# Kernel tuning notes

Hardware: AMD Instinct MI355X
Metric: run time of the kernel (lower is better)

## Reference

```python
import jax, jax.numpy as jnp
import numpy as np

B, C, H, W = 4, 256, 64, 64
D = C // 8  # query/key projection dim


def setup_inputs() -> dict:
    key = jax.random.key(0)
    ks = jax.random.split(key, 8)
    s = 0.02
    return {
        "x": jax.random.normal(ks[0], (B, C, H, W), dtype=jnp.float32),
        "Wq": jax.random.normal(ks[1], (D, C), dtype=jnp.float32) * s,
        "bq": jax.random.normal(ks[2], (D,), dtype=jnp.float32) * s,
        "Wk": jax.random.normal(ks[3], (D, C), dtype=jnp.float32) * s,
        "bk": jax.random.normal(ks[4], (D,), dtype=jnp.float32) * s,
        "Wv": jax.random.normal(ks[5], (C, C), dtype=jnp.float32) * s,
        "bv": jax.random.normal(ks[6], (C,), dtype=jnp.float32) * s,
        "gamma": jax.random.normal(ks[7], (1,), dtype=jnp.float32),
    }


def reference(x, Wq, bq, Wk, bk, Wv, bv, gamma):
    b, c, h, w = x.shape
    n = h * w
    xf = x.reshape(b, c, n)                                  # B,C,N
    # 1x1 convs == per-pixel linear projections
    q = jnp.einsum("dc,bcn->bdn", Wq, xf) + bq[None, :, None]  # B,D,N
    k = jnp.einsum("dc,bcn->bdn", Wk, xf) + bk[None, :, None]  # B,D,N
    v = jnp.einsum("ec,bcn->ben", Wv, xf) + bv[None, :, None]  # B,C,N
    # energy[b,i,j] = <q[:, i], k[:, j]>  (query index i, key index j)
    energy = jnp.einsum("bdi,bdj->bij", q, k)                # B,N,N
    attention = jax.nn.softmax(energy, axis=-1)              # softmax over keys j
    # out[b,c,i] = sum_j v[b,c,j] * attention[b,i,j]
    out = jnp.einsum("bcj,bij->bci", v, attention)           # B,C,N
    out = out.reshape(b, c, h, w)
    return gamma[0] * out + x
```

## Files before the change

### kernel.cpp

```cpp
#include <hip/hip_runtime.h>
#include <hip/hip_bf16.h>
#include <cstdint>

#define B_ 4
#define C_ 256
#define N_ 4096
#define D_ 32

typedef __attribute__((ext_vector_type(8))) short bf16x8;
typedef __attribute__((ext_vector_type(4))) short s16x4;
typedef __attribute__((ext_vector_type(4))) float f32x4;

__device__ inline unsigned short f2bf(float f) {
    union { float f; uint32_t u; } v; v.f = f;
    uint32_t u = v.u;
    u += 0x7FFFu + ((u >> 16) & 1u);
    return (unsigned short)(u >> 16);
}

__global__ __launch_bounds__(256) void wconv_kernel(
    const float* __restrict__ Wq, const float* __restrict__ Wk,
    const float* __restrict__ Wv, unsigned short* __restrict__ Wb)
{
    int i = (blockIdx.x * 256 + threadIdx.x) * 4;
    int r = i >> 8, k = i & 255;
    const float* src = (r < 32) ? Wq + r * 256 + k
                     : (r < 64) ? Wk + (r - 32) * 256 + k
                                : Wv + (r - 64) * 256 + k;
    f32x4 v = *reinterpret_cast<const f32x4*>(src);
    s16x4 o;
    #pragma unroll
    for (int j = 0; j < 4; ++j) o[j] = (short)f2bf(v[j]);
    *reinterpret_cast<s16x4*>(Wb + i) = o;
}

__global__ __launch_bounds__(256) void proj_kernel(
    const float* __restrict__ x, const unsigned short* __restrict__ Wb,
    const float* __restrict__ bq, const float* __restrict__ bk,
    const float* __restrict__ bv,
    unsigned short* __restrict__ Qt, unsigned short* __restrict__ Kt,
    unsigned short* __restrict__ V)
{
    __shared__ __align__(16) char smem[32768];
    const int t  = threadIdx.x;
    const int w  = t >> 6;
    const int l  = t & 63;
    const int lg = l >> 4;
    const int ll = l & 15;
    const int n0 = blockIdx.x * 64;
    const int b  = blockIdx.y;

    #pragma unroll
    for (int rep = 0; rep < 16; ++rep) {
        int flat = rep * 256 + t;
        int c = flat >> 4, chunk = flat & 15;
        f32x4 xv = *reinterpret_cast<const f32x4*>(
            x + ((size_t)(b * C_ + c)) * N_ + n0 + chunk * 4);
        #pragma unroll
        for (int j = 0; j < 4; ++j) {
            int n = chunk * 4 + j;
            *reinterpret_cast<unsigned short*>(
                smem + n * 512 + ((c * 2) ^ ((n & 7) << 4))) = f2bf(xv[j]);
        }
    }

    bf16x8 Af[5], Afn[5];
    #pragma unroll
    for (int rt = 0; rt < 5; ++rt) {
        int r = w * 80 + rt * 16 + ll;
        Af[rt] = *reinterpret_cast<const bf16x8*>(Wb + r * 256 + lg * 8);
    }

    f32x4 acc[5][4];
    #pragma unroll
    for (int rt = 0; rt < 5; ++rt)
        #pragma unroll
        for (int nt = 0; nt < 4; ++nt) acc[rt][nt] = (f32x4){0.f, 0.f, 0.f, 0.f};

    __syncthreads();

    for (int kc = 0; kc < 8; ++kc) {
        if (kc < 7) {
            #pragma unroll
            for (int rt = 0; rt < 5; ++rt) {
                int r = w * 80 + rt * 16 + ll;
                Afn[rt] = *reinterpret_cast<const bf16x8*>(
                    Wb + r * 256 + (kc + 1) * 32 + lg * 8);
            }
        }
        bf16x8 Bf[4];
        #pragma unroll
        for (int nt = 0; nt < 4; ++nt) {
            int n = nt * 16 + ll;
            Bf[nt] = *reinterpret_cast<const bf16x8*>(
                smem + n * 512 + ((kc * 64 + lg * 16) ^ ((n & 7) << 4)));
        }
        #pragma unroll
        for (int rt = 0; rt < 5; ++rt)
            #pragma unroll
            for (int nt = 0; nt < 4; ++nt)
                acc[rt][nt] = __builtin_amdgcn_mfma_f32_16x16x32_bf16(
                    Af[rt], Bf[nt], acc[rt][nt], 0, 0, 0);
        if (kc < 7) {
            #pragma unroll
            for (int rt = 0; rt < 5; ++rt) Af[rt] = Afn[rt];
        }
    }

    #pragma unroll
    for (int rt = 0; rt < 5; ++rt) {
        const int rrow = w * 80 + rt * 16 + lg * 4;
        float bias[4];
        #pragma unroll
        for (int q = 0; q < 4; ++q) {
            int rg = rrow + q;
            bias[q] = (rg < 32) ? bq[rg] : (rg < 64) ? bk[rg - 32] : bv[rg - 64];
        }
        if (rrow < 64) {
            const int d0 = rrow & 31;
            unsigned short* dst = (rrow < 32) ? Qt : Kt;
            #pragma unroll
            for (int nt = 0; nt < 4; ++nt) {
                int n = n0 + nt * 16 + ll;
                s16x4 sv;
                #pragma unroll
                for (int q = 0; q < 4; ++q)
                    sv[q] = (short)f2bf(acc[rt][nt][q] + bias[q]);
                *reinterpret_cast<s16x4*>(dst + ((size_t)b * N_ + n) * D_ + d0) = sv;
            }
        } else {
            #pragma unroll
            for (int nt = 0; nt < 4; ++nt) {
                int n = n0 + nt * 16 + ll;
                #pragma unroll
                for (int q = 0; q < 4; ++q) {
                    int c = rrow - 64 + q;
                    V[((size_t)(b * C_ + c)) * N_ + n] = f2bf(acc[rt][nt][q] + bias[q]);
                }
            }
        }
    }
}

__device__ inline void stageV(const unsigned short* __restrict__ Vg, int b,
                              int c0, int j0, char* VsBuf, int w, int l) {
    #pragma unroll
    for (int i = 0; i < 2; ++i) {
        const int Lbyte = i * 8192 + w * 1024 + l * 16;
        const int c   = Lbyte >> 7;
        const int off = Lbyte & 127;
        const int src_off = off ^ ((c & 7) << 4);
        const unsigned short* src =
            Vg + ((size_t)(b * C_ + c0 + c)) * N_ + j0 + (src_off >> 1);
        char* dst = VsBuf + i * 8192 + w * 1024;
        __builtin_amdgcn_global_load_lds(
            (const __attribute__((address_space(1))) uint32_t*)src,
            (__attribute__((address_space(3))) uint32_t*)dst, 16, 0, 0);
    }
}

__global__ __launch_bounds__(512) void attn_kernel(
    const unsigned short* __restrict__ Qt, const unsigned short* __restrict__ Kt,
    const unsigned short* __restrict__ Vg, const float* __restrict__ x,
    const float* __restrict__ gamma, float* __restrict__ out)
{
    __shared__ __align__(16) char smem[49664];
    char* Pbase = smem + 32768;
    float* LbufF = reinterpret_cast<float*>(smem + 49152);
    const int t  = threadIdx.x;
    const int w  = t >> 6;
    const int l  = t & 63;
    const int lg = l >> 4;
    const int ll = l & 15;
    const int qg = w >> 2;
    const int ch = w & 3;
    const int qr = w >> 1;
    const int jcb = (w & 1) * 2;
    const int n0 = (blockIdx.x >> 1) * 64;
    const int c0 = (blockIdx.x & 1) * 128;
    const int b  = blockIdx.y;

    const bf16x8 qfrag = *reinterpret_cast<const bf16x8*>(
        Qt + ((size_t)b * N_ + n0 + qr * 16 + ll) * D_ + 8 * lg);

    f32x4 acc[2][2];
    #pragma unroll
    for (int qt = 0; qt < 2; ++qt)
        #pragma unroll
        for (int ct = 0; ct < 2; ++ct) acc[qt][ct] = (f32x4){0.f, 0.f, 0.f, 0.f};
    float l_lane[4] = {0.f, 0.f, 0.f, 0.f};

    stageV(Vg, b, c0, 0, smem, w, l);
    bf16x8 kcur[2], knxt[2];
    #pragma unroll
    for (int s = 0; s < 2; ++s)
        kcur[s] = *reinterpret_cast<const bf16x8*>(
            Kt + ((size_t)b * N_ + (jcb + s) * 16 + ll) * D_ + 8 * lg);

    const f32x4 zero4 = {0.f, 0.f, 0.f, 0.f};

    for (int kt = 0; kt < 64; ++kt) {
        const int buf = kt & 1;
        const int ktn = (kt < 63) ? kt + 1 : 63;

        #pragma unroll
        for (int s = 0; s < 2; ++s)
            knxt[s] = *reinterpret_cast<const bf16x8*>(
                Kt + ((size_t)b * N_ + ktn * 64 + (jcb + s) * 16 + ll) * D_ + 8 * lg);

        f32x4 sf[2];
        #pragma unroll
        for (int s = 0; s < 2; ++s)
            sf[s] = __builtin_amdgcn_mfma_f32_16x16x32_bf16(qfrag, kcur[s], zero4, 0, 0, 0);

        float pv[2][4];
        #pragma unroll
        for (int s = 0; s < 2; ++s)
            #pragma unroll
            for (int r = 0; r < 4; ++r) {
                float p = __expf(fminf(sf[s][r], 60.f));
                pv[s][r] = p;
                l_lane[r] += p;
            }

        char* Pw = Pbase + buf * 8192;
        #pragma unroll
        for (int s = 0; s < 2; ++s)
            #pragma unroll
            for (int r = 0; r < 4; ++r) {
                int row = qr * 16 + lg * 4 + r;
                int col = (jcb + s) * 16 + ll;
                *reinterpret_cast<unsigned short*>(
                    Pw + row * 128 + ((col * 2) ^ ((row & 7) << 4))) = f2bf(pv[s][r]);
            }

        asm volatile("s_waitcnt lgkmcnt(0)" ::: "memory");
        asm volatile("s_waitcnt vmcnt(2)" ::: "memory");
        __builtin_amdgcn_s_barrier();
        asm volatile("" ::: "memory");

        if (kt < 63)
            stageV(Vg, b, c0, ktn * 64, smem + (buf ^ 1) * 16384, w, l);

        char* Pr = Pbase + buf * 8192;
        bf16x8 pfrag[2][2];
        #pragma unroll
        for (int qt = 0; qt < 2; ++qt)
            #pragma unroll
            for (int kh = 0; kh < 2; ++kh) {
                int row = qg * 32 + qt * 16 + ll;
                pfrag[qt][kh] = *reinterpret_cast<const bf16x8*>(
                    Pr + row * 128 + ((kh * 64 + lg * 16) ^ ((row & 7) << 4)));
            }
        char* Vs = smem + buf * 16384;
        #pragma unroll
        for (int ct = 0; ct < 2; ++ct) {
            int cl = ch * 32 + ct * 16 + ll;
            #pragma unroll
            for (int kh = 0; kh < 2; ++kh) {
                bf16x8 vf = *reinterpret_cast<const bf16x8*>(
                    Vs + cl * 128 + ((kh * 64 + lg * 16) ^ ((cl & 7) << 4)));
                #pragma unroll
                for (int qt = 0; qt < 2; ++qt)
                    acc[qt][ct] = __builtin_amdgcn_mfma_f32_16x16x32_bf16(
                        pfrag[qt][kh], vf, acc[qt][ct], 0, 0, 0);
            }
        }

        #pragma unroll
        for (int s = 0; s < 2; ++s) kcur[s] = knxt[s];
    }

    #pragma unroll
    for (int off = 1; off < 16; off <<= 1)
        #pragma unroll
        for (int r = 0; r < 4; ++r)
            l_lane[r] += __shfl_xor(l_lane[r], off);
    if (ll == 0) {
        #pragma unroll
        for (int r = 0; r < 4; ++r) LbufF[w * 16 + lg * 4 + r] = l_lane[r];
    }
    __syncthreads();

    float inv[2][4];
    #pragma unroll
    for (int qt = 0; qt < 2; ++qt)
        #pragma unroll
        for (int r = 0; r < 4; ++r) {
            int qrow = qg * 2 + qt;
            int lq = lg * 4 + r;
            float ls = LbufF[(2 * qrow) * 16 + lq] + LbufF[(2 * qrow + 1) * 16 + lq];
            inv[qt][r] = 1.f / ls;
        }

    #pragma unroll
    for (int qt = 0; qt < 2; ++qt)
        #pragma unroll
        for (int ct = 0; ct < 2; ++ct) {
            int cl = ch * 32 + ct * 16 + ll;
            int ncol = qg * 32 + qt * 16 + lg * 4;
            f32x4 v;
            #pragma unroll
            for (int r = 0; r < 4; ++r) v[r] = acc[qt][ct][r] * inv[qt][r];
            *reinterpret_cast<f32x4*>(smem + cl * 256 + ((ncol * 4) ^ ((cl & 7) << 4))) = v;
        }
    __syncthreads();

    const float g0 = gamma[0];
    #pragma unroll
    for (int p = 0; p < 4; ++p) {
        int li = p * 512 + t;
        int cl = li >> 4;
        int n4 = (li & 15) * 4;
        f32x4 ov = *reinterpret_cast<const f32x4*>(
            smem + cl * 256 + ((n4 * 4) ^ ((cl & 7) << 4)));
        size_t gi = ((size_t)(b * C_ + c0 + cl)) * N_ + n0 + n4;
        f32x4 xv = *reinterpret_cast<const f32x4*>(x + gi);
        f32x4 res;
        #pragma unroll
        for (int j = 0; j < 4; ++j) res[j] = g0 * ov[j] + xv[j];
        *reinterpret_cast<f32x4*>(out + gi) = res;
    }
}

extern "C" void kernel_launch(void* const* d_in, const int* in_sizes, int n_in,
                              void* d_out, int out_size, void* d_ws, size_t ws_size,
                              hipStream_t stream) {
    const float* x     = (const float*)d_in[0];
    const float* Wq    = (const float*)d_in[1];
    const float* bq    = (const float*)d_in[2];
    const float* Wk    = (const float*)d_in[3];
    const float* bk    = (const float*)d_in[4];
    const float* Wv    = (const float*)d_in[5];
    const float* bv    = (const float*)d_in[6];
    const float* gamma = (const float*)d_in[7];
    float* out = (float*)d_out;

    char* ws = (char*)d_ws;
    unsigned short* Qt = (unsigned short*)(ws);
    unsigned short* Kt = (unsigned short*)(ws + (1u << 20));
    unsigned short* V  = (unsigned short*)(ws + (2u << 20));
    unsigned short* Wb = (unsigned short*)(ws + (10u << 20));

    wconv_kernel<<<dim3(80), 256, 0, stream>>>(Wq, Wk, Wv, Wb);
    proj_kernel<<<dim3(N_ / 64, B_), 256, 0, stream>>>(
        x, Wb, bq, bk, bv, Qt, Kt, V);
    attn_kernel<<<dim3(2 * N_ / 64, B_), 512, 0, stream>>>(
        Qt, Kt, V, x, gamma, out);
}
```

Baseline: 161.5 us.

## Retile attention to 32 queries by all channels, fold log2e into Q

The attention kernel now gives each block 32 query rows and all 256 channels instead of 64 queries and half the channels. QK^T and softmax are therefore computed once per query tile rather than twice, with each wave handling one 16-key column and 32 output channels. Q is prescaled by log2(e) in the projection so the softmax can use raw v_exp_f32, and the PV MFMA section runs under a raised s_setprio. The projection tile is halved to 32 pixels. In exchange, the attention kernel uses more LDS for the full-channel V double buffer, which may reduce occupancy.

```diff
diff --git a/kernel.cpp b/kernel.cpp
--- a/kernel.cpp
+++ b/kernel.cpp
@@ -6,6 +6,7 @@
 #define C_ 256
 #define N_ 4096
 #define D_ 32
+#define LOG2E 1.44269504088896f
 
 typedef __attribute__((ext_vector_type(8))) short bf16x8;
 typedef __attribute__((ext_vector_type(4))) short s16x4;
@@ -16,6 +17,12 @@
     uint32_t u = v.u;
     u += 0x7FFFu + ((u >> 16) & 1u);
     return (unsigned short)(u >> 16);
+}
+
+__device__ inline float exp2_raw(float x) {
+    float r;
+    asm("v_exp_f32 %0, %1" : "=v"(r) : "v"(x));
+    return r;
 }
 
 __global__ __launch_bounds__(256) void wconv_kernel(
@@ -41,19 +48,19 @@
     unsigned short* __restrict__ Qt, unsigned short* __restrict__ Kt,
     unsigned short* __restrict__ V)
 {
-    __shared__ __align__(16) char smem[32768];
+    __shared__ __align__(16) char smem[16384];
     const int t  = threadIdx.x;
     const int w  = t >> 6;
     const int l  = t & 63;
     const int lg = l >> 4;
     const int ll = l & 15;
-    const int n0 = blockIdx.x * 64;
+    const int n0 = blockIdx.x * 32;
     const int b  = blockIdx.y;
 
     #pragma unroll
-    for (int rep = 0; rep < 16; ++rep) {
+    for (int rep = 0; rep < 8; ++rep) {
         int flat = rep * 256 + t;
-        int c = flat >> 4, chunk = flat & 15;
+        int c = flat >> 3, chunk = flat & 7;
         f32x4 xv = *reinterpret_cast<const f32x4*>(
             x + ((size_t)(b * C_ + c)) * N_ + n0 + chunk * 4);
         #pragma unroll
@@ -71,11 +78,11 @@
         Af[rt] = *reinterpret_cast<const bf16x8*>(Wb + r * 256 + lg * 8);
     }
 
-    f32x4 acc[5][4];
+    f32x4 acc[5][2];
     #pragma unroll
     for (int rt = 0; rt < 5; ++rt)
         #pragma unroll
-        for (int nt = 0; nt < 4; ++nt) acc[rt][nt] = (f32x4){0.f, 0.f, 0.f, 0.f};
+        for (int nt = 0; nt < 2; ++nt) acc[rt][nt] = (f32x4){0.f, 0.f, 0.f, 0.f};
 
     __syncthreads();
 
@@ -88,9 +95,9 @@
                     Wb + r * 256 + (kc + 1) * 32 + lg * 8);
             }
         }
-        bf16x8 Bf[4];
-        #pragma unroll
-        for (int nt = 0; nt < 4; ++nt) {
+        bf16x8 Bf[2];
+        #pragma unroll
+        for (int nt = 0; nt < 2; ++nt) {
             int n = nt * 16 + ll;
             Bf[nt] = *reinterpret_cast<const bf16x8*>(
                 smem + n * 512 + ((kc * 64 + lg * 16) ^ ((n & 7) << 4)));
@@ -98,7 +105,7 @@
         #pragma unroll
         for (int rt = 0; rt < 5; ++rt)
             #pragma unroll
-            for (int nt = 0; nt < 4; ++nt)
+            for (int nt = 0; nt < 2; ++nt)
                 acc[rt][nt] = __builtin_amdgcn_mfma_f32_16x16x32_bf16(
                     Af[rt], Bf[nt], acc[rt][nt], 0, 0, 0);
         if (kc < 7) {
@@ -118,19 +125,23 @@
         }
         if (rrow < 64) {
             const int d0 = rrow & 31;
-            unsigned short* dst = (rrow < 32) ? Qt : Kt;
-            #pragma unroll
-            for (int nt = 0; nt < 4; ++nt) {
+            const bool isQ = (rrow < 32);
+            unsigned short* dst = isQ ? Qt : Kt;
+            #pragma unroll
+            for (int nt = 0; nt < 2; ++nt) {
                 int n = n0 + nt * 16 + ll;
                 s16x4 sv;
                 #pragma unroll
-                for (int q = 0; q < 4; ++q)
-                    sv[q] = (short)f2bf(acc[rt][nt][q] + bias[q]);
+                for (int q = 0; q < 4; ++q) {
+                    float v = acc[rt][nt][q] + bias[q];
+                    if (isQ) v *= LOG2E;
+                    sv[q] = (short)f2bf(v);
+                }
                 *reinterpret_cast<s16x4*>(dst + ((size_t)b * N_ + n) * D_ + d0) = sv;
             }
         } else {
             #pragma unroll
-            for (int nt = 0; nt < 4; ++nt) {
+            for (int nt = 0; nt < 2; ++nt) {
                 int n = n0 + nt * 16 + ll;
                 #pragma unroll
                 for (int q = 0; q < 4; ++q) {
@@ -143,15 +154,15 @@
 }
 
 __device__ inline void stageV(const unsigned short* __restrict__ Vg, int b,
-                              int c0, int j0, char* VsBuf, int w, int l) {
-    #pragma unroll
-    for (int i = 0; i < 2; ++i) {
+                              int j0, char* VsBuf, int w, int l) {
+    #pragma unroll
+    for (int i = 0; i < 4; ++i) {
         const int Lbyte = i * 8192 + w * 1024 + l * 16;
         const int c   = Lbyte >> 7;
         const int off = Lbyte & 127;
         const int src_off = off ^ ((c & 7) << 4);
         const unsigned short* src =
-            Vg + ((size_t)(b * C_ + c0 + c)) * N_ + j0 + (src_off >> 1);
+            Vg + ((size_t)(b * C_ + c)) * N_ + j0 + (src_off >> 1);
         char* dst = VsBuf + i * 8192 + w * 1024;
         __builtin_amdgcn_global_load_lds(
             (const __attribute__((address_space(1))) uint32_t*)src,
@@ -164,24 +175,21 @@
     const unsigned short* __restrict__ Vg, const float* __restrict__ x,
     const float* __restrict__ gamma, float* __restrict__ out)
 {
-    __shared__ __align__(16) char smem[49664];
-    char* Pbase = smem + 32768;
-    float* LbufF = reinterpret_cast<float*>(smem + 49152);
+    __shared__ __align__(16) char smem[74240];
+    char* Pbase = smem + 65536;
+    float* LbufF = reinterpret_cast<float*>(smem + 73728);
     const int t  = threadIdx.x;
     const int w  = t >> 6;
     const int l  = t & 63;
     const int lg = l >> 4;
     const int ll = l & 15;
-    const int qg = w >> 2;
-    const int ch = w & 3;
-    const int qr = w >> 1;
-    const int jcb = (w & 1) * 2;
-    const int n0 = (blockIdx.x >> 1) * 64;
-    const int c0 = (blockIdx.x & 1) * 128;
+    const int qt_p = w >> 2;
+    const int jc   = w & 3;
+    const int n0 = blockIdx.x * 32;
     const int b  = blockIdx.y;
 
     const bf16x8 qfrag = *reinterpret_cast<const bf16x8*>(
-        Qt + ((size_t)b * N_ + n0 + qr * 16 + ll) * D_ + 8 * lg);
+        Qt + ((size_t)b * N_ + n0 + qt_p * 16 + ll) * D_ + 8 * lg);
 
     f32x4 acc[2][2];
     #pragma unroll
@@ -190,12 +198,9 @@
         for (int ct = 0; ct < 2; ++ct) acc[qt][ct] = (f32x4){0.f, 0.f, 0.f, 0.f};
     float l_lane[4] = {0.f, 0.f, 0.f, 0.f};
 
-    stageV(Vg, b, c0, 0, smem, w, l);
-    bf16x8 kcur[2], knxt[2];
-    #pragma unroll
-    for (int s = 0; s < 2; ++s)
-        kcur[s] = *reinterpret_cast<const bf16x8*>(
-            Kt + ((size_t)b * N_ + (jcb + s) * 16 + ll) * D_ + 8 * lg);
+    stageV(Vg, b, 0, smem, w, l);
+    bf16x8 kcur = *reinterpret_cast<const bf16x8*>(
+        Kt + ((size_t)b * N_ + jc * 16 + ll) * D_ + 8 * lg);
 
     const f32x4 zero4 = {0.f, 0.f, 0.f, 0.f};
 
@@ -203,59 +208,51 @@
         const int buf = kt & 1;
         const int ktn = (kt < 63) ? kt + 1 : 63;
 
-        #pragma unroll
-        for (int s = 0; s < 2; ++s)
-            knxt[s] = *reinterpret_cast<const bf16x8*>(
-                Kt + ((size_t)b * N_ + ktn * 64 + (jcb + s) * 16 + ll) * D_ + 8 * lg);
-
-        f32x4 sf[2];
-        #pragma unroll
-        for (int s = 0; s < 2; ++s)
-            sf[s] = __builtin_amdgcn_mfma_f32_16x16x32_bf16(qfrag, kcur[s], zero4, 0, 0, 0);
-
-        float pv[2][4];
-        #pragma unroll
-        for (int s = 0; s < 2; ++s)
-            #pragma unroll
-            for (int r = 0; r < 4; ++r) {
-                float p = __expf(fminf(sf[s][r], 60.f));
-                pv[s][r] = p;
-                l_lane[r] += p;
-            }
-
-        char* Pw = Pbase + buf * 8192;
-        #pragma unroll
-        for (int s = 0; s < 2; ++s)
-            #pragma unroll
-            for (int r = 0; r < 4; ++r) {
-                int row = qr * 16 + lg * 4 + r;
-                int col = (jcb + s) * 16 + ll;
-                *reinterpret_cast<unsigned short*>(
-                    Pw + row * 128 + ((col * 2) ^ ((row & 7) << 4))) = f2bf(pv[s][r]);
-            }
+        bf16x8 knxt = *reinterpret_cast<const bf16x8*>(
+            Kt + ((size_t)b * N_ + ktn * 64 + jc * 16 + ll) * D_ + 8 * lg);
+
+        f32x4 sf = __builtin_amdgcn_mfma_f32_16x16x32_bf16(qfrag, kcur, zero4, 0, 0, 0);
+
+        float pv[4];
+        #pragma unroll
+        for (int r = 0; r < 4; ++r) {
+            float p = exp2_raw(fminf(sf[r], 86.f));
+            pv[r] = p;
+            l_lane[r] += p;
+        }
+
+        char* Pw = Pbase + buf * 4096;
+        #pragma unroll
+        for (int r = 0; r < 4; ++r) {
+            int row = qt_p * 16 + lg * 4 + r;
+            int col = jc * 16 + ll;
+            *reinterpret_cast<unsigned short*>(
+                Pw + row * 128 + ((col * 2) ^ ((row & 7) << 4))) = f2bf(pv[r]);
+        }
 
         asm volatile("s_waitcnt lgkmcnt(0)" ::: "memory");
-        asm volatile("s_waitcnt vmcnt(2)" ::: "memory");
+        asm volatile("s_waitcnt vmcnt(1)" ::: "memory");
         __builtin_amdgcn_s_barrier();
         asm volatile("" ::: "memory");
 
         if (kt < 63)
-            stageV(Vg, b, c0, ktn * 64, smem + (buf ^ 1) * 16384, w, l);
-
-        char* Pr = Pbase + buf * 8192;
+            stageV(Vg, b, ktn * 64, smem + (buf ^ 1) * 32768, w, l);
+
+        char* Pr = Pbase + buf * 4096;
         bf16x8 pfrag[2][2];
         #pragma unroll
         for (int qt = 0; qt < 2; ++qt)
             #pragma unroll
             for (int kh = 0; kh < 2; ++kh) {
-                int row = qg * 32 + qt * 16 + ll;
+                int row = qt * 16 + ll;
                 pfrag[qt][kh] = *reinterpret_cast<const bf16x8*>(
                     Pr + row * 128 + ((kh * 64 + lg * 16) ^ ((row & 7) << 4)));
             }
-        char* Vs = smem + buf * 16384;
+        char* Vs = smem + buf * 32768;
+        __builtin_amdgcn_s_setprio(1);
         #pragma unroll
         for (int ct = 0; ct < 2; ++ct) {
-            int cl = ch * 32 + ct * 16 + ll;
+            int cl = w * 32 + ct * 16 + ll;
             #pragma unroll
             for (int kh = 0; kh < 2; ++kh) {
                 bf16x8 vf = *reinterpret_cast<const bf16x8*>(
@@ -266,9 +263,9 @@
                         pfrag[qt][kh], vf, acc[qt][ct], 0, 0, 0);
             }
         }
-
-        #pragma unroll
-        for (int s = 0; s < 2; ++s) kcur[s] = knxt[s];
+        __builtin_amdgcn_s_setprio(0);
+
+        kcur = knxt;
     }
 
     #pragma unroll
@@ -287,9 +284,9 @@
     for (int qt = 0; qt < 2; ++qt)
         #pragma unroll
         for (int r = 0; r < 4; ++r) {
-            int qrow = qg * 2 + qt;
             int lq = lg * 4 + r;
-            float ls = LbufF[(2 * qrow) * 16 + lq] + LbufF[(2 * qrow + 1) * 16 + lq];
+            float ls = LbufF[(qt * 4 + 0) * 16 + lq] + LbufF[(qt * 4 + 1) * 16 + lq]
+                     + LbufF[(qt * 4 + 2) * 16 + lq] + LbufF[(qt * 4 + 3) * 16 + lq];
             inv[qt][r] = 1.f / ls;
         }
 
@@ -297,12 +294,12 @@
     for (int qt = 0; qt < 2; ++qt)
         #pragma unroll
         for (int ct = 0; ct < 2; ++ct) {
-            int cl = ch * 32 + ct * 16 + ll;
-            int ncol = qg * 32 + qt * 16 + lg * 4;
+            int cl = w * 32 + ct * 16 + ll;
+            int ncol = qt * 16 + lg * 4;
             f32x4 v;
             #pragma unroll
             for (int r = 0; r < 4; ++r) v[r] = acc[qt][ct][r] * inv[qt][r];
-            *reinterpret_cast<f32x4*>(smem + cl * 256 + ((ncol * 4) ^ ((cl & 7) << 4))) = v;
+            *reinterpret_cast<f32x4*>(smem + cl * 128 + ((ncol * 4) ^ ((cl & 7) << 4))) = v;
         }
     __syncthreads();
 
@@ -310,11 +307,11 @@
     #pragma unroll
     for (int p = 0; p < 4; ++p) {
         int li = p * 512 + t;
-        int cl = li >> 4;
-        int n4 = (li & 15) * 4;
+        int cl = li >> 3;
+        int n4 = (li & 7) * 4;
         f32x4 ov = *reinterpret_cast<const f32x4*>(
-            smem + cl * 256 + ((n4 * 4) ^ ((cl & 7) << 4)));
-        size_t gi = ((size_t)(b * C_ + c0 + cl)) * N_ + n0 + n4;
+            smem + cl * 128 + ((n4 * 4) ^ ((cl & 7) << 4)));
+        size_t gi = ((size_t)(b * C_ + cl)) * N_ + n0 + n4;
         f32x4 xv = *reinterpret_cast<const f32x4*>(x + gi);
         f32x4 res;
         #pragma unroll
@@ -343,8 +340,8 @@
     unsigned short* Wb = (unsigned short*)(ws + (10u << 20));
 
     wconv_kernel<<<dim3(80), 256, 0, stream>>>(Wq, Wk, Wv, Wb);
-    proj_kernel<<<dim3(N_ / 64, B_), 256, 0, stream>>>(
+    proj_kernel<<<dim3(N_ / 32, B_), 256, 0, stream>>>(
         x, Wb, bq, bk, bv, Qt, Kt, V);
-    attn_kernel<<<dim3(2 * N_ / 64, B_), 512, 0, stream>>>(
+    attn_kernel<<<dim3(N_ / 32, B_), 512, 0, stream>>>(
         Qt, Kt, V, x, gamma, out);
 }
```

Result: no change. 160.2 us (-0.8%).
